# Performance work log

Hardware: AMD Instinct MI355X
Metric: run time of the kernel (lower is better)

Reference implementation:

```python
import jax, jax.numpy as jnp
import numpy as np

H = 6            # nheads
DPH = 200.0      # dim_per_head buffer = mha_dimension / nheads (used as divisor, NOT sqrt)
EPS = 1e-5


def layernorm(x, g, b):
    m = jnp.mean(x, axis=-1, keepdims=True)
    v = jnp.mean((x - m) ** 2, axis=-1, keepdims=True)
    return (x - m) * jax.lax.rsqrt(v + EPS) * g + b


def leaky(x):
    # torch.nn.LeakyReLU(True) -> negative_slope = 1.0 (identity), kept for faithfulness
    return jnp.where(x >= 0, x, 1.0 * x)


def setup_inputs() -> dict:
    key = jax.random.key(0)
    ks = jax.random.split(key, 16)
    B, L, D, M = 4, 2048, 512, 1200
    s_in = 1.0 / np.sqrt(D)
    s_m = 1.0 / np.sqrt(M)
    return {
        "query": jax.random.normal(ks[0], (B, L, D), jnp.float32),
        "keyval": jax.random.normal(ks[1], (B, 1, D), jnp.float32),
        "Wq": jax.random.normal(ks[2], (D, M), jnp.float32) * s_in,
        "bq": jnp.zeros((M,), jnp.float32),
        "Wkv": jax.random.normal(ks[3], (D, 2 * M), jnp.float32) * s_in,
        "bkv": jnp.zeros((2 * M,), jnp.float32),
        "Wff": jax.random.normal(ks[4], (M, D), jnp.float32) * s_m,
        "bff": jnp.zeros((D,), jnp.float32),
        "g1": jnp.ones((D,), jnp.float32),
        "b1": jnp.zeros((D,), jnp.float32),
        "W2a": jax.random.normal(ks[5], (D, 4 * D), jnp.float32) * s_in,
        "b2a": jnp.zeros((4 * D,), jnp.float32),
        "W2b": jax.random.normal(ks[6], (4 * D, D), jnp.float32) / np.sqrt(4 * D),
        "b2b": jnp.zeros((D,), jnp.float32),
        "g2": jnp.ones((D,), jnp.float32),
        "b2": jnp.zeros((D,), jnp.float32),
    }


def reference(query, keyval, Wq, bq, Wkv, bkv, Wff, bff, g1, b1,
              W2a, b2a, W2b, b2b, g2, b2):
    B, L, D = query.shape
    kv = jnp.broadcast_to(keyval, query.shape)           # keyval.expand_as(query)
    Q = query @ Wq + bq                                  # [B,L,M]
    KV = kv @ Wkv + bkv                                  # [B,L,2M]
    K, V = jnp.split(KV, 2, axis=-1)

    def heads(x):  # b l (h d) -> b h l d
        return x.reshape(B, L, H, -1).transpose(0, 2, 1, 3)

    Qh, Kh, Vh = heads(Q), heads(K), heads(V)
    logits = jnp.einsum('bhid,bhjd->bhij', Qh, Kh) / DPH  # note: / d, not / sqrt(d)
    sm = jax.nn.softmax(logits, axis=-1)                  # [B,H,L,L]
    mha = jnp.einsum('bhij,bhjd->bhid', sm, Vh)
    mha_ = mha.transpose(0, 2, 1, 3).reshape(B, L, -1)    # b h i d -> b i (h d)

    out = mha_ @ Wff + bff                                # dropout = identity (eval)
    out_ = layernorm(out + query, g1, b1)
    out2 = leaky(out_ @ W2a + b2a) @ W2b + b2b
    out3 = layernorm(out_ + out2, g2, b2)
    out3 = out3 + kv
    return out3, sm
```

## Files before the change

kernel.cpp:

```cpp
#include <hip/hip_runtime.h>
#include <hip/hip_bf16.h>


typedef __bf16 bf16x8 __attribute__((ext_vector_type(8)));
typedef float f32x4 __attribute__((ext_vector_type(4)));

constexpr size_t OUT3_N = 4ull * 2048 * 512;
constexpr size_t SM_N4  = (4ull * 6 * 2048 * 2048) / 4;
constexpr float  SMV    = 1.0f / 2048.0f;

constexpr size_t S1 = 0,        C1 = 6291456;
constexpr size_t S2 = 6291456,  C2 = 4194304;
constexpr size_t S3 = 10485760, C3 = 6291456;
constexpr size_t S4 = 16777216, C4 = 3145728;
constexpr size_t S5 = 19922944, C5 = 2621440;
constexpr size_t S6 = 22544384, C6 = 2621440;
static_assert(S6 + C6 == SM_N4, "fill slices must cover sm");

__device__ inline void fill_slice(f32x4* __restrict__ p, size_t base, size_t cnt,
                                  int fb, int nfb){
    const f32x4 v = { SMV, SMV, SMV, SMV };
    const size_t stride = (size_t)nfb * 256;
    for (size_t j = (size_t)fb * 256 + threadIdx.x; j < cnt; j += stride)
        __builtin_nontemporal_store(v, p + base + j);
}

template<bool ATOMIC>
__device__ void gemm_tile(const __bf16* __restrict__ A, const __bf16* __restrict__ BT,
                          float* __restrict__ C, int Ndim, int Kdim,
                          int bm, int bn, int k0beg, int k0end){
    __shared__ __bf16 As[64 * 64];
    __shared__ __bf16 Bs[64 * 64];
    const int tid = threadIdx.x, wave = tid >> 6, lane = tid & 63;
    const int r_st = wave * 8 + (lane >> 3);
    const int c8g  = (lane & 7) ^ (r_st & 7);
    const __bf16* Ag = A  + (size_t)(bm + r_st) * Kdim + c8g * 8;
    const __bf16* Bg = BT + (size_t)(bn + r_st) * Kdim + c8g * 8;
    const size_t rowskip = (size_t)32 * Kdim;
    const int wm = (wave >> 1) * 32, wn = (wave & 1) * 32;
    const int lm = lane & 15, lq = lane >> 4;
    f32x4 acc[2][2] = {};
    for (int k0 = k0beg; k0 < k0end; k0 += 64){
        __builtin_amdgcn_global_load_lds(
            (const __attribute__((address_space(1))) void*)(Ag + k0),
            (__attribute__((address_space(3))) void*)&As[wave * 512], 16, 0, 0);
        __builtin_amdgcn_global_load_lds(
            (const __attribute__((address_space(1))) void*)(Ag + k0 + rowskip),
            (__attribute__((address_space(3))) void*)&As[2048 + wave * 512], 16, 0, 0);
        __builtin_amdgcn_global_load_lds(
            (const __attribute__((address_space(1))) void*)(Bg + k0),
            (__attribute__((address_space(3))) void*)&Bs[wave * 512], 16, 0, 0);
        __builtin_amdgcn_global_load_lds(
            (const __attribute__((address_space(1))) void*)(Bg + k0 + rowskip),
            (__attribute__((address_space(3))) void*)&Bs[2048 + wave * 512], 16, 0, 0);
        __syncthreads();
        #pragma unroll
        for (int kb = 0; kb < 64; kb += 32){
            const int sw = (((kb >> 3) + lq) ^ (lm & 7)) << 3;
            bf16x8 a0 = *(const bf16x8*)&As[(wm + lm) * 64 + sw];
            bf16x8 a1 = *(const bf16x8*)&As[(wm + 16 + lm) * 64 + sw];
            bf16x8 b0 = *(const bf16x8*)&Bs[(wn + lm) * 64 + sw];
            bf16x8 b1 = *(const bf16x8*)&Bs[(wn + 16 + lm) * 64 + sw];
            acc[0][0] = __builtin_amdgcn_mfma_f32_16x16x32_bf16(a0, b0, acc[0][0], 0, 0, 0);
            acc[0][1] = __builtin_amdgcn_mfma_f32_16x16x32_bf16(a0, b1, acc[0][1], 0, 0, 0);
            acc[1][0] = __builtin_amdgcn_mfma_f32_16x16x32_bf16(a1, b0, acc[1][0], 0, 0, 0);
            acc[1][1] = __builtin_amdgcn_mfma_f32_16x16x32_bf16(a1, b1, acc[1][1], 0, 0, 0);
        }
        __syncthreads();
    }
    #pragma unroll
    for (int mi = 0; mi < 2; ++mi)
      #pragma unroll
      for (int ni = 0; ni < 2; ++ni)
        #pragma unroll
        for (int r = 0; r < 4; ++r){
            int row = bm + wm + mi * 16 + lq * 4 + r;
            int col = bn + wn + ni * 16 + lm;
            if (ATOMIC) atomicAdd(&C[(size_t)row * Ndim + col], acc[mi][ni][r]);
            else        C[(size_t)row * Ndim + col] = acc[mi][ni][r];
        }
}

__global__ __launch_bounds__(256) void k1_prep_kv(const float* __restrict__ W2a,
        const float* __restrict__ b2a, __bf16* __restrict__ A1,
        const float* __restrict__ W2b, __bf16* __restrict__ W2bT,
        const float* __restrict__ keyval, const float* __restrict__ Wkv,
        const float* __restrict__ bkv, float* __restrict__ V, f32x4* __restrict__ smf){
    __shared__ float sh[32 * 33];
    const int bid = blockIdx.x, tid = threadIdx.x;
    if (bid < 1152){
        int r = bid >> 1;
        int c = (bid & 1) * 1024 + tid * 4;
        float4 v;
        if (r < 512)       v = *(const float4*)(W2a + (size_t)r * 2048 + c);
        else if (r == 512) v = *(const float4*)(b2a + c);
        else               v = make_float4(0.f, 0.f, 0.f, 0.f);
        __bf16* o = A1 + (size_t)r * 2048 + c;
        o[0] = (__bf16)v.x; o[1] = (__bf16)v.y; o[2] = (__bf16)v.z; o[3] = (__bf16)v.w;
    } else if (bid < 2176){
        int t = bid - 1152;
        int c0 = (t & 15) * 32, r0 = (t >> 4) * 32;
        int tx = tid & 31, ty = tid >> 5;
        for (int i = ty; i < 32; i += 8)
            sh[i * 33 + tx] = W2b[(size_t)(r0 + i) * 512 + c0 + tx];
        __syncthreads();
        for (int i = ty; i < 32; i += 8)
            W2bT[(size_t)(c0 + i) * 2048 + r0 + tx] = (__bf16)sh[tx * 33 + i];
    } else if (bid < 2336){
        int i = bid - 2176;
        int b = i & 3, mc = (i >> 2) % 5, kc = i / 20;
        int m = mc * 256 + tid;
        if (m < 1200){
            float acc = (kc == 0) ? bkv[1200 + m] : 0.f;
            const float* kvb = keyval + (size_t)b * 512;
            int d0 = kc * 64;
            #pragma unroll 8
            for (int d = d0; d < d0 + 64; ++d)
                acc += kvb[d] * Wkv[(size_t)d * 2400 + 1200 + m];
            atomicAdd(&V[b * 1200 + m], acc);
        }
    } else {
        fill_slice(smf, S1, C1, bid - 2336, 512);
    }
}

__global__ __launch_bounds__(256) void k2_oc(const float* __restrict__ V,
        const float* __restrict__ Wff, const float* __restrict__ bff,
        float* __restrict__ oc, f32x4* __restrict__ smf){
    const int bid = blockIdx.x, tid = threadIdx.x;
    if (bid < 96){
        int b = bid & 3, jc = (bid >> 2) & 1, kc = bid >> 3;
        int j = jc * 256 + tid;
        float acc = (kc == 0) ? bff[j] : 0.f;
        const float* vb = V + b * 1200;
        int m0 = kc * 100;
        #pragma unroll 5
        for (int m = m0; m < m0 + 100; ++m)
            acc += vb[m] * Wff[(size_t)m * 512 + j];
        atomicAdd(&oc[b * 512 + j], acc);
    } else {
        fill_slice(smf, S2, C2, bid - 96, 512);
    }
}

__global__ __launch_bounds__(256) void k3_fold(const __bf16* __restrict__ A1,
        const __bf16* __restrict__ W2bT, float* __restrict__ Wf, f32x4* __restrict__ smf){
    const int bid = blockIdx.x;
    if (bid < 288){
        int tile = bid % 72, kc = bid / 72;
        int tm = tile % 9, tn = tile / 9;
        gemm_tile<true>(A1, W2bT, Wf, 512, 2048, tm * 64, tn * 64, kc * 512, (kc + 1) * 512);
    } else {
        fill_slice(smf, S3, C3, bid - 288, 512);
    }
}

__global__ __launch_bounds__(256) void k4_ln1_tcast(const float* __restrict__ q,
        const float* __restrict__ oc, const float* __restrict__ g1,
        const float* __restrict__ b1, __bf16* __restrict__ Xb,
        const float* __restrict__ Wf, __bf16* __restrict__ WfT, f32x4* __restrict__ smf){
    __shared__ float sh[32 * 33];
    const int bid = blockIdx.x, t = threadIdx.x;
    if (bid < 8192){
        const int b = bid >> 11;
        const size_t base = (size_t)bid * 512;
        float2 qv = *(const float2*)(q + base + 2 * t);
        float2 ov = *(const float2*)(oc + (size_t)b * 512 + 2 * t);
        float v0 = qv.x + ov.x, v1 = qv.y + ov.y;
        float s = v0 + v1, ss = v0 * v0 + v1 * v1;
        for (int off = 32; off; off >>= 1){ s += __shfl_down(s, off); ss += __shfl_down(ss, off); }
        int wv = t >> 6, ln = t & 63;
        if (ln == 0){ sh[wv] = s; sh[4 + wv] = ss; }
        __syncthreads();
        if (t == 0){
            float S  = sh[0] + sh[1] + sh[2] + sh[3];
            float SS = sh[4] + sh[5] + sh[6] + sh[7];
            float m = S * (1.0f / 512.0f);
            float var = SS * (1.0f / 512.0f) - m * m;
            sh[0] = m; sh[1] = rsqrtf(var + 1e-5f);
        }
        __syncthreads();
        float m = sh[0], r = sh[1];
        float2 gv = *(const float2*)(g1 + 2 * t);
        float2 bv = *(const float2*)(b1 + 2 * t);
        union { __bf16 h[2]; unsigned u; } pk;
        pk.h[0] = (__bf16)((v0 - m) * r * gv.x + bv.x);
        pk.h[1] = (__bf16)((v1 - m) * r * gv.y + bv.y);
        *(unsigned*)(Xb + base + 2 * t) = pk.u;
    } else if (bid < 8448){
        int tt = bid - 8192;
        int c0 = (tt & 15) * 32, r0 = (tt >> 4) * 32;
        int tx = t & 31, ty = t >> 5;
        for (int i = ty; i < 32; i += 8)
            sh[i * 33 + tx] = Wf[(size_t)(r0 + i) * 512 + c0 + tx];
        __syncthreads();
        for (int i = ty; i < 32; i += 8)
            WfT[(size_t)(c0 + i) * 512 + r0 + tx] = (__bf16)sh[tx * 33 + i];
    } else {
        fill_slice(smf, S4, C4, bid - 8448, 512);
    }
}

__global__ __launch_bounds__(256) void k5_gemm(const __bf16* __restrict__ X,
        const __bf16* __restrict__ WfT, float* __restrict__ out2, f32x4* __restrict__ smf){
    const int bid = blockIdx.x;
    if (bid < 1024){
        gemm_tile<false>(X, WfT, out2, 512, 512, (bid >> 3) * 64, (bid & 7) * 64, 0, 512);
    } else {
        fill_slice(smf, S5, C5, bid - 1024, 512);
    }
}

__global__ __launch_bounds__(256) void k6_ln2(const __bf16* __restrict__ X,
        const float* __restrict__ o2, const float* __restrict__ bfrow,
        const float* __restrict__ b2b, const float* __restrict__ g2,
        const float* __restrict__ b2, const float* __restrict__ keyval,
        float* __restrict__ out3, f32x4* __restrict__ smf){
    __shared__ float sh[8];
    const int bid = blockIdx.x, t = threadIdx.x;
    if (bid < 8192){
        const int b = bid >> 11;
        const size_t base = (size_t)bid * 512;
        union { unsigned u; __bf16 h[2]; } xv;
        xv.u = *(const unsigned*)(X + base + 2 * t);
        float2 cv = *(const float2*)(o2 + base + 2 * t);
        float f0 = bfrow[2 * t] + b2b[2 * t], f1 = bfrow[2 * t + 1] + b2b[2 * t + 1];
        float v0 = (float)xv.h[0] + cv.x + f0, v1 = (float)xv.h[1] + cv.y + f1;
        float s = v0 + v1, ss = v0 * v0 + v1 * v1;
        for (int off = 32; off; off >>= 1){ s += __shfl_down(s, off); ss += __shfl_down(ss, off); }
        int wv = t >> 6, ln = t & 63;
        if (ln == 0){ sh[wv] = s; sh[4 + wv] = ss; }
        __syncthreads();
        if (t == 0){
            float S  = sh[0] + sh[1] + sh[2] + sh[3];
            float SS = sh[4] + sh[5] + sh[6] + sh[7];
            float m = S * (1.0f / 512.0f);
            float var = SS * (1.0f / 512.0f) - m * m;
            sh[0] = m; sh[1] = rsqrtf(var + 1e-5f);
        }
        __syncthreads();
        float m = sh[0], r = sh[1];
        float2 gv = *(const float2*)(g2 + 2 * t);
        float2 bv = *(const float2*)(b2 + 2 * t);
        float2 kv = *(const float2*)(keyval + (size_t)b * 512 + 2 * t);
        float y0 = (v0 - m) * r * gv.x + bv.x + kv.x;
        float y1 = (v1 - m) * r * gv.y + bv.y + kv.y;
        *(float2*)(out3 + base + 2 * t) = make_float2(y0, y1);
    } else {
        fill_slice(smf, S6, C6, bid - 8192, 512);
    }
}

extern "C" void kernel_launch(void* const* d_in, const int* in_sizes, int n_in,
                              void* d_out, int out_size, void* d_ws, size_t ws_size,
                              hipStream_t stream){
    const float* query  = (const float*)d_in[0];
    const float* keyval = (const float*)d_in[1];
    const float* Wkv = (const float*)d_in[4];
    const float* bkv = (const float*)d_in[5];
    const float* Wff = (const float*)d_in[6];
    const float* bff = (const float*)d_in[7];
    const float* g1  = (const float*)d_in[8];
    const float* b1  = (const float*)d_in[9];
    const float* W2a = (const float*)d_in[10];
    const float* b2a = (const float*)d_in[11];
    const float* W2b = (const float*)d_in[12];
    const float* b2b = (const float*)d_in[13];
    const float* g2  = (const float*)d_in[14];
    const float* b2  = (const float*)d_in[15];

    float* out3 = (float*)d_out;
    f32x4* smf  = (f32x4*)(out3 + OUT3_N);

    char* base = (ws_size >= (64ull << 20)) ? (char*)d_ws : (char*)smf;
    float*  t_Wf   = (float*)base;
    float*  t_V    = t_Wf + 294912;
    float*  t_oc   = t_V + 4800;
    float*  t_out2 = t_oc + 2048;
    __bf16* t_A1   = (__bf16*)(t_out2 + 4194304);
    __bf16* t_W2bT = t_A1 + 1179648;
    __bf16* t_WfT  = t_W2bT + 1048576;
    __bf16* t_X    = t_WfT + 262144;

    (void)hipMemsetAsync(t_Wf, 0, (294912 + 4800 + 2048) * sizeof(float), stream);
    k1_prep_kv<<<2848, 256, 0, stream>>>(W2a, b2a, t_A1, W2b, t_W2bT,
                                         keyval, Wkv, bkv, t_V, smf);
    k2_oc<<<608, 256, 0, stream>>>(t_V, Wff, bff, t_oc, smf);
    k3_fold<<<800, 256, 0, stream>>>(t_A1, t_W2bT, t_Wf, smf);
    k4_ln1_tcast<<<8960, 256, 0, stream>>>(query, t_oc, g1, b1, t_X, t_Wf, t_WfT, smf);
    k5_gemm<<<1536, 256, 0, stream>>>(t_X, t_WfT, t_out2, smf);
    k6_ln2<<<8704, 256, 0, stream>>>(t_X, t_out2, t_Wf + 262144, b2b, g2, b2,
                                     keyval, out3, smf);
}
```

Before: 501.2 us.

## Fold Wkv_V·Wff into a weight product and merge prep kernels into five launches

Computes a folded 512x512 weight WF2 = Wkv[:,V]·Wff and bias bF2 in the first kernel, so the per-batch constant attention output is a single keyval·WF2 product. This removes one kernel launch by merging the old V and oc stages into the fold and prep kernels, and rebalances the softmax fill slices across five kernels. It adds a 512x1200x512 fp32 GEMM with atomics that is more arithmetic than the old vector products, in exchange for one fewer dependent launch.

```diff
diff --git a/kernel.cpp b/kernel.cpp
--- a/kernel.cpp
+++ b/kernel.cpp
@@ -9,13 +9,12 @@
 constexpr size_t SM_N4  = (4ull * 6 * 2048 * 2048) / 4;
 constexpr float  SMV    = 1.0f / 2048.0f;
 
-constexpr size_t S1 = 0,        C1 = 6291456;
-constexpr size_t S2 = 6291456,  C2 = 4194304;
-constexpr size_t S3 = 10485760, C3 = 6291456;
-constexpr size_t S4 = 16777216, C4 = 3145728;
-constexpr size_t S5 = 19922944, C5 = 2621440;
-constexpr size_t S6 = 22544384, C6 = 2621440;
-static_assert(S6 + C6 == SM_N4, "fill slices must cover sm");
+constexpr size_t SA = 0,        CA = 6815744;
+constexpr size_t SB = 6815744,  CB = 5636096;
+constexpr size_t SC = 12451840, CC = 4456448;
+constexpr size_t SD = 16908288, CD = 4128768;
+constexpr size_t SE = 21037056, CE = 4128768;
+static_assert(SE + CE == SM_N4, "fill slices must cover sm");
 
 __device__ inline void fill_slice(f32x4* __restrict__ p, size_t base, size_t cnt,
                                   int fb, int nfb){
@@ -81,11 +80,49 @@
         }
 }
 
-__global__ __launch_bounds__(256) void k1_prep_kv(const float* __restrict__ W2a,
+__device__ void wf2_tile(const float* __restrict__ Wkv, const float* __restrict__ Wff,
+                         float* __restrict__ WF2, int tm, int tn, int kc){
+    __shared__ float As2[64][17];
+    __shared__ float Bs2[16][64];
+    const int t = threadIdx.x;
+    const int ar = t >> 2, ac = (t & 3) * 4;
+    const int br = t >> 4, bc = (t & 15) * 4;
+    const int ti = t >> 4, tj = t & 15;
+    float acc[4][4] = {};
+    const int d0 = tm * 64, j0 = tn * 64, m0 = kc * 240;
+    for (int s = 0; s < 15; ++s){
+        int mb = m0 + s * 16;
+        float4 av = *(const float4*)(Wkv + (size_t)(d0 + ar) * 2400 + 1200 + mb + ac);
+        float4 bv = *(const float4*)(Wff + (size_t)(mb + br) * 512 + j0 + bc);
+        As2[ar][ac] = av.x; As2[ar][ac + 1] = av.y; As2[ar][ac + 2] = av.z; As2[ar][ac + 3] = av.w;
+        *(float4*)&Bs2[br][bc] = bv;
+        __syncthreads();
+        #pragma unroll
+        for (int kk = 0; kk < 16; ++kk){
+            float a0 = As2[ti * 4 + 0][kk], a1 = As2[ti * 4 + 1][kk];
+            float a2 = As2[ti * 4 + 2][kk], a3 = As2[ti * 4 + 3][kk];
+            float b0 = Bs2[kk][tj * 4 + 0], b1 = Bs2[kk][tj * 4 + 1];
+            float b2 = Bs2[kk][tj * 4 + 2], b3 = Bs2[kk][tj * 4 + 3];
+            acc[0][0] += a0 * b0; acc[0][1] += a0 * b1; acc[0][2] += a0 * b2; acc[0][3] += a0 * b3;
+            acc[1][0] += a1 * b0; acc[1][1] += a1 * b1; acc[1][2] += a1 * b2; acc[1][3] += a1 * b3;
+            acc[2][0] += a2 * b0; acc[2][1] += a2 * b1; acc[2][2] += a2 * b2; acc[2][3] += a2 * b3;
+            acc[3][0] += a3 * b0; acc[3][1] += a3 * b1; acc[3][2] += a3 * b2; acc[3][3] += a3 * b3;
+        }
+        __syncthreads();
+    }
+    #pragma unroll
+    for (int i = 0; i < 4; ++i)
+      #pragma unroll
+      for (int j = 0; j < 4; ++j)
+        atomicAdd(&WF2[(size_t)(d0 + ti * 4 + i) * 512 + j0 + tj * 4 + j], acc[i][j]);
+}
+
+__global__ __launch_bounds__(256) void kA(const float* __restrict__ W2a,
         const float* __restrict__ b2a, __bf16* __restrict__ A1,
         const float* __restrict__ W2b, __bf16* __restrict__ W2bT,
-        const float* __restrict__ keyval, const float* __restrict__ Wkv,
-        const float* __restrict__ bkv, float* __restrict__ V, f32x4* __restrict__ smf){
+        const float* __restrict__ Wkv, const float* __restrict__ Wff,
+        const float* __restrict__ bkv, const float* __restrict__ bff,
+        float* __restrict__ WF2, float* __restrict__ bF2, f32x4* __restrict__ smf){
     __shared__ float sh[32 * 33];
     const int bid = blockIdx.x, tid = threadIdx.x;
     if (bid < 1152){
@@ -106,56 +143,49 @@
         __syncthreads();
         for (int i = ty; i < 32; i += 8)
             W2bT[(size_t)(c0 + i) * 2048 + r0 + tx] = (__bf16)sh[tx * 33 + i];
-    } else if (bid < 2336){
+    } else if (bid < 2496){
         int i = bid - 2176;
-        int b = i & 3, mc = (i >> 2) % 5, kc = i / 20;
-        int m = mc * 256 + tid;
-        if (m < 1200){
-            float acc = (kc == 0) ? bkv[1200 + m] : 0.f;
-            const float* kvb = keyval + (size_t)b * 512;
-            int d0 = kc * 64;
-            #pragma unroll 8
-            for (int d = d0; d < d0 + 64; ++d)
-                acc += kvb[d] * Wkv[(size_t)d * 2400 + 1200 + m];
-            atomicAdd(&V[b * 1200 + m], acc);
-        }
-    } else {
-        fill_slice(smf, S1, C1, bid - 2336, 512);
-    }
-}
-
-__global__ __launch_bounds__(256) void k2_oc(const float* __restrict__ V,
-        const float* __restrict__ Wff, const float* __restrict__ bff,
-        float* __restrict__ oc, f32x4* __restrict__ smf){
+        int tile = i & 63, kc = i >> 6;
+        wf2_tile(Wkv, Wff, WF2, tile >> 3, tile & 7, kc);
+    } else if (bid < 2506){
+        int i = bid - 2496;
+        int j = (i & 1) * 256 + tid, kc = i >> 1;
+        float acc = (kc == 0) ? bff[j] : 0.f;
+        int m0 = kc * 240;
+        for (int m = m0; m < m0 + 240; ++m)
+            acc += bkv[1200 + m] * Wff[(size_t)m * 512 + j];
+        atomicAdd(&bF2[j], acc);
+    } else {
+        fill_slice(smf, SA, CA, bid - 2506, 512);
+    }
+}
+
+__global__ __launch_bounds__(256) void kB(const __bf16* __restrict__ A1,
+        const __bf16* __restrict__ W2bT, float* __restrict__ Wf,
+        const float* __restrict__ keyval, const float* __restrict__ WF2,
+        const float* __restrict__ bF2, float* __restrict__ oc, f32x4* __restrict__ smf){
     const int bid = blockIdx.x, tid = threadIdx.x;
-    if (bid < 96){
-        int b = bid & 3, jc = (bid >> 2) & 1, kc = bid >> 3;
-        int j = jc * 256 + tid;
-        float acc = (kc == 0) ? bff[j] : 0.f;
-        const float* vb = V + b * 1200;
-        int m0 = kc * 100;
-        #pragma unroll 5
-        for (int m = m0; m < m0 + 100; ++m)
-            acc += vb[m] * Wff[(size_t)m * 512 + j];
-        atomicAdd(&oc[b * 512 + j], acc);
-    } else {
-        fill_slice(smf, S2, C2, bid - 96, 512);
-    }
-}
-
-__global__ __launch_bounds__(256) void k3_fold(const __bf16* __restrict__ A1,
-        const __bf16* __restrict__ W2bT, float* __restrict__ Wf, f32x4* __restrict__ smf){
-    const int bid = blockIdx.x;
     if (bid < 288){
         int tile = bid % 72, kc = bid / 72;
-        int tm = tile % 9, tn = tile / 9;
-        gemm_tile<true>(A1, W2bT, Wf, 512, 2048, tm * 64, tn * 64, kc * 512, (kc + 1) * 512);
-    } else {
-        fill_slice(smf, S3, C3, bid - 288, 512);
-    }
-}
-
-__global__ __launch_bounds__(256) void k4_ln1_tcast(const float* __restrict__ q,
+        gemm_tile<true>(A1, W2bT, Wf, 512, 2048, (tile % 9) * 64, (tile / 9) * 64,
+                        kc * 512, (kc + 1) * 512);
+    } else if (bid < 320){
+        int i = bid - 288;
+        int b = i & 3, jc = (i >> 2) & 1, kc = i >> 3;
+        int j = jc * 256 + tid;
+        float acc = (kc == 0) ? bF2[j] : 0.f;
+        const float* kvb = keyval + (size_t)b * 512;
+        int d0 = kc * 128;
+        #pragma unroll 8
+        for (int d = d0; d < d0 + 128; ++d)
+            acc += kvb[d] * WF2[(size_t)d * 512 + j];
+        atomicAdd(&oc[b * 512 + j], acc);
+    } else {
+        fill_slice(smf, SB, CB, bid - 320, 512);
+    }
+}
+
+__global__ __launch_bounds__(256) void kC(const float* __restrict__ q,
         const float* __restrict__ oc, const float* __restrict__ g1,
         const float* __restrict__ b1, __bf16* __restrict__ Xb,
         const float* __restrict__ Wf, __bf16* __restrict__ WfT, f32x4* __restrict__ smf){
@@ -197,21 +227,21 @@
         for (int i = ty; i < 32; i += 8)
             WfT[(size_t)(c0 + i) * 512 + r0 + tx] = (__bf16)sh[tx * 33 + i];
     } else {
-        fill_slice(smf, S4, C4, bid - 8448, 512);
-    }
-}
-
-__global__ __launch_bounds__(256) void k5_gemm(const __bf16* __restrict__ X,
+        fill_slice(smf, SC, CC, bid - 8448, 512);
+    }
+}
+
+__global__ __launch_bounds__(256) void kD(const __bf16* __restrict__ X,
         const __bf16* __restrict__ WfT, float* __restrict__ out2, f32x4* __restrict__ smf){
     const int bid = blockIdx.x;
     if (bid < 1024){
         gemm_tile<false>(X, WfT, out2, 512, 512, (bid >> 3) * 64, (bid & 7) * 64, 0, 512);
     } else {
-        fill_slice(smf, S5, C5, bid - 1024, 512);
-    }
-}
-
-__global__ __launch_bounds__(256) void k6_ln2(const __bf16* __restrict__ X,
+        fill_slice(smf, SD, CD, bid - 1024, 512);
+    }
+}
+
+__global__ __launch_bounds__(256) void kE(const __bf16* __restrict__ X,
         const float* __restrict__ o2, const float* __restrict__ bfrow,
         const float* __restrict__ b2b, const float* __restrict__ g2,
         const float* __restrict__ b2, const float* __restrict__ keyval,
@@ -247,7 +277,7 @@
         float y1 = (v1 - m) * r * gv.y + bv.y + kv.y;
         *(float2*)(out3 + base + 2 * t) = make_float2(y0, y1);
     } else {
-        fill_slice(smf, S6, C6, bid - 8192, 512);
+        fill_slice(smf, SE, CE, bid - 8192, 512);
     }
 }
 
@@ -273,22 +303,22 @@
     f32x4* smf  = (f32x4*)(out3 + OUT3_N);
 
     char* base = (ws_size >= (64ull << 20)) ? (char*)d_ws : (char*)smf;
-    float*  t_Wf   = (float*)base;
-    float*  t_V    = t_Wf + 294912;
-    float*  t_oc   = t_V + 4800;
+    float*  t_WF2  = (float*)base;
+    float*  t_bF2  = t_WF2 + 262144;
+    float*  t_Wf   = t_bF2 + 512;
+    float*  t_oc   = t_Wf + 294912;
     float*  t_out2 = t_oc + 2048;
     __bf16* t_A1   = (__bf16*)(t_out2 + 4194304);
     __bf16* t_W2bT = t_A1 + 1179648;
     __bf16* t_WfT  = t_W2bT + 1048576;
     __bf16* t_X    = t_WfT + 262144;
 
-    (void)hipMemsetAsync(t_Wf, 0, (294912 + 4800 + 2048) * sizeof(float), stream);
-    k1_prep_kv<<<2848, 256, 0, stream>>>(W2a, b2a, t_A1, W2b, t_W2bT,
-                                         keyval, Wkv, bkv, t_V, smf);
-    k2_oc<<<608, 256, 0, stream>>>(t_V, Wff, bff, t_oc, smf);
-    k3_fold<<<800, 256, 0, stream>>>(t_A1, t_W2bT, t_Wf, smf);
-    k4_ln1_tcast<<<8960, 256, 0, stream>>>(query, t_oc, g1, b1, t_X, t_Wf, t_WfT, smf);
-    k5_gemm<<<1536, 256, 0, stream>>>(t_X, t_WfT, t_out2, smf);
-    k6_ln2<<<8704, 256, 0, stream>>>(t_X, t_out2, t_Wf + 262144, b2b, g2, b2,
-                                     keyval, out3, smf);
-}
+    (void)hipMemsetAsync(t_WF2, 0, 559616 * sizeof(float), stream);
+    kA<<<3018, 256, 0, stream>>>(W2a, b2a, t_A1, W2b, t_W2bT, Wkv, Wff, bkv, bff,
+                                 t_WF2, t_bF2, smf);
+    kB<<<832, 256, 0, stream>>>(t_A1, t_W2bT, t_Wf, keyval, t_WF2, t_bF2, t_oc, smf);
+    kC<<<8960, 256, 0, stream>>>(query, t_oc, g1, b1, t_X, t_Wf, t_WfT, smf);
+    kD<<<1536, 256, 0, stream>>>(t_X, t_WfT, t_out2, smf);
+    kE<<<8704, 256, 0, stream>>>(t_X, t_out2, t_Wf + 262144, b2b, g2, b2,
+                                 keyval, out3, smf);
+}
```

Result: slower. 560.9 us (+11.9%).
